# Kernel tuning notes

Measured on AMD Instinct MI355X. Metric: run time of the kernel, lower is better.

## Reference

```python
import jax, jax.numpy as jnp
import numpy as np

D_MODEL = 1024
NUM_HEADS = 16
HEAD_DIM = D_MODEL // NUM_HEADS


def setup_inputs() -> dict:
    key = jax.random.key(0)
    ks = jax.random.split(key, 11)
    B, S = 2, 2048
    s = 1.0 / np.sqrt(D_MODEL)
    return {
        "q": jax.random.normal(ks[0], (B, S, D_MODEL), jnp.float32),
        "k": jax.random.normal(ks[1], (B, S, D_MODEL), jnp.float32),
        "v": jax.random.normal(ks[2], (B, S, D_MODEL), jnp.float32),
        "Wq": jax.random.normal(ks[3], (D_MODEL, D_MODEL), jnp.float32) * s,
        "bq": jnp.zeros((D_MODEL,), jnp.float32),
        "Wk": jax.random.normal(ks[4], (D_MODEL, D_MODEL), jnp.float32) * s,
        "bk": jnp.zeros((D_MODEL,), jnp.float32),
        "Wv": jax.random.normal(ks[5], (D_MODEL, D_MODEL), jnp.float32) * s,
        "bv": jnp.zeros((D_MODEL,), jnp.float32),
        "Wo": jax.random.normal(ks[6], (D_MODEL, D_MODEL), jnp.float32) * s,
        "bo": jnp.zeros((D_MODEL,), jnp.float32),
    }


def _split_heads(x):
    B, S, _ = x.shape
    return x.reshape(B, S, NUM_HEADS, HEAD_DIM).transpose(0, 2, 1, 3)  # [B,H,S,Dh]


def reference(q, k, v, Wq, bq, Wk, bk, Wv, bv, Wo, bo):
    B, S, _ = q.shape
    qh = _split_heads(q @ Wq.T + bq)
    kh = _split_heads(k @ Wk.T + bk)
    vh = _split_heads(v @ Wv.T + bv)
    scale = 1.0 / jnp.sqrt(jnp.asarray(HEAD_DIM, qh.dtype))
    scores = jnp.einsum("bhqd,bhkd->bhqk", qh, kh) * scale  # [B,H,S,S]
    attn = jax.nn.softmax(scores, axis=-1)
    out = jnp.einsum("bhqk,bhkd->bhqd", attn, vh)
    out = out.transpose(0, 2, 1, 3).reshape(B, S, D_MODEL)
    return out @ Wo.T + bo
```

## Files before the change

### kernel.cpp

```cpp
#include <hip/hip_runtime.h>
#include <cstdint>
#include <cstddef>

#define DEVI __device__ __forceinline__

typedef short bf16x8 __attribute__((ext_vector_type(8)));
typedef short bf16x4 __attribute__((ext_vector_type(4)));
typedef float f32x4 __attribute__((ext_vector_type(4)));
typedef float f32x16 __attribute__((ext_vector_type(16)));
typedef unsigned short u16x4 __attribute__((ext_vector_type(4)));

constexpr int D_MODEL = 1024;
constexpr int HEADS = 16;
constexpr int DH = 64;
constexpr int SEQ = 2048;
constexpr int KDIM = 1024;

DEVI unsigned short f2bf(float f) {
  union { float f; unsigned u; } v; v.f = f;
  unsigned r = v.u + 0x7fffu + ((v.u >> 16) & 1u);
  return (unsigned short)(r >> 16);
}

DEVI unsigned pkbf(float a, float b) {
  return __builtin_amdgcn_perm(__float_as_uint(b), __float_as_uint(a), 0x07060302u);
}

DEVI void cp16(const void* g, void* l) {
  __builtin_amdgcn_global_load_lds(
      (const __attribute__((address_space(1))) void*)g,
      (__attribute__((address_space(3))) void*)l, 16, 0, 0);
}

#define BAR()        asm volatile("s_barrier" ::: "memory")
#define WAITVM(n)    asm volatile("s_waitcnt vmcnt(" #n ")" ::: "memory")

__global__ void __launch_bounds__(256) castall(
    const float* __restrict__ q, const float* __restrict__ k, const float* __restrict__ v,
    const float* __restrict__ Wq, const float* __restrict__ Wk,
    const float* __restrict__ Wv, const float* __restrict__ Wo,
    unsigned short* __restrict__ qb, unsigned short* __restrict__ kb, unsigned short* __restrict__ vb,
    unsigned short* __restrict__ Wqb, unsigned short* __restrict__ Wkb,
    unsigned short* __restrict__ Wvb, unsigned short* __restrict__ Wob) {
  int bid = blockIdx.x;
  const float* s; unsigned short* d; int off;
  if (bid < 12288) {
    int w = bid >> 12; off = bid & 4095;
    s = (w == 0) ? q : ((w == 1) ? k : v);
    d = (w == 0) ? qb : ((w == 1) ? kb : vb);
  } else {
    int w = (bid - 12288) >> 10; off = bid & 1023;
    s = (w == 0) ? Wq : ((w == 1) ? Wk : ((w == 2) ? Wv : Wo));
    d = (w == 0) ? Wqb : ((w == 1) ? Wkb : ((w == 2) ? Wvb : Wob));
  }
  int i = (off * 256 + threadIdx.x) * 4;
  float4 x = *(const float4*)(s + i);
  u16x4 o; o[0] = f2bf(x.x); o[1] = f2bf(x.y); o[2] = f2bf(x.z); o[3] = f2bf(x.w);
  *(u16x4*)(d + i) = o;
}

__global__ void __launch_bounds__(256) qkv_gemm(
    const unsigned short* __restrict__ qb, const unsigned short* __restrict__ kb,
    const unsigned short* __restrict__ vb,
    const unsigned short* __restrict__ Wqb, const unsigned short* __restrict__ Wkb,
    const unsigned short* __restrict__ Wvb,
    const float* __restrict__ bq, const float* __restrict__ bk, const float* __restrict__ bv,
    unsigned short* __restrict__ Qh, unsigned short* __restrict__ Kh,
    unsigned short* __restrict__ Vt, float qscale) {
  __shared__ unsigned short As[3][128 * 32];
  __shared__ unsigned short Bs[3][128 * 32];
  const int bid = blockIdx.x, seg = bid >> 8, inner = bid & 255;
  const int bm = inner & 31, bn = inner >> 5;
  const unsigned short* A = (seg == 0) ? qb : ((seg == 1) ? kb : vb);
  const unsigned short* W = (seg == 0) ? Wqb : ((seg == 1) ? Wkb : Wvb);
  const float* bias = (seg == 0) ? bq : ((seg == 1) ? bk : bv);
  unsigned short* O = (seg == 0) ? Qh : ((seg == 1) ? Kh : Vt);
  const float oscale = (seg == 0) ? qscale : 1.0f;
  const int mode = (seg == 2) ? 1 : 0;

  const int tid = threadIdx.x, lane = tid & 63, wave = tid >> 6;
  const int l16 = lane & 15, quad = lane >> 4;
  const int wm = (wave >> 1) * 64, wn = (wave & 1) * 64;
  const int sw = (l16 >> 1) & 3;
  f32x4 acc[4][4] = {};

  const int r0 = tid >> 2, p0 = tid & 3;
  const int c0 = (p0 ^ ((r0 >> 1) & 3)) * 8;
  const int r1 = (256 + tid) >> 2;
  const int c1 = (p0 ^ ((r1 >> 1) & 3)) * 8;
  const unsigned short* Arow0 = A + (size_t)(bm * 128 + r0) * KDIM + c0;
  const unsigned short* Arow1 = A + (size_t)(bm * 128 + r1) * KDIM + c1;
  const unsigned short* Wrow0 = W + (size_t)(bn * 128 + r0) * KDIM + c0;
  const unsigned short* Wrow1 = W + (size_t)(bn * 128 + r1) * KDIM + c1;

#define QKV_ISSUE(K0, P)                                    \
  do {                                                      \
    cp16(Arow0 + (K0), &As[P][tid * 8]);                    \
    cp16(Arow1 + (K0), &As[P][(256 + tid) * 8]);            \
    cp16(Wrow0 + (K0), &Bs[P][tid * 8]);                    \
    cp16(Wrow1 + (K0), &Bs[P][(256 + tid) * 8]);            \
  } while (0)

#define QKV_COMPUTE(P)                                                             \
  do {                                                                             \
    bf16x8 af[4], bfr[4];                                                          \
    _Pragma("unroll") for (int t = 0; t < 4; ++t)                                  \
        af[t] = *(const bf16x8*)&As[P][(wm + t * 16 + l16) * 32 + ((quad ^ sw) * 8)]; \
    _Pragma("unroll") for (int t = 0; t < 4; ++t)                                  \
        bfr[t] = *(const bf16x8*)&Bs[P][(wn + t * 16 + l16) * 32 + ((quad ^ sw) * 8)]; \
    _Pragma("unroll") for (int i = 0; i < 4; ++i)                                  \
        _Pragma("unroll") for (int j = 0; j < 4; ++j)                              \
            acc[i][j] = __builtin_amdgcn_mfma_f32_16x16x32_bf16(af[i], bfr[j],     \
                                                                acc[i][j], 0, 0, 0); \
  } while (0)

  QKV_ISSUE(0, 0);
  QKV_ISSUE(32, 1);
  for (int k = 0; k < 30; k += 3) {
    BAR(); QKV_ISSUE((k + 2) * 32, 2); WAITVM(8); BAR(); QKV_COMPUTE(0);
    BAR(); QKV_ISSUE((k + 3) * 32, 0); WAITVM(8); BAR(); QKV_COMPUTE(1);
    BAR(); QKV_ISSUE((k + 4) * 32, 1); WAITVM(8); BAR(); QKV_COMPUTE(2);
  }
  WAITVM(4); BAR(); QKV_COMPUTE(0);
  WAITVM(0); BAR(); QKV_COMPUTE(1);

#pragma unroll
  for (int i = 0; i < 4; ++i) {
#pragma unroll
    for (int j = 0; j < 4; ++j) {
      const int col = bn * 128 + wn + j * 16 + l16;
      const float bv = bias[col];
#pragma unroll
      for (int r = 0; r < 4; ++r) {
        const int row = bm * 128 + wm + i * 16 + quad * 4 + r;
        const float val = (acc[i][j][r] + bv) * oscale;
        const int b = row >> 11, s = row & (SEQ - 1);
        const int h = col >> 6, d = col & (DH - 1);
        size_t idx;
        if (mode == 0) idx = ((size_t)(b * HEADS + h) * SEQ + s) * DH + d;
        else           idx = ((size_t)(b * HEADS + h) * DH + d) * SEQ + s;
        O[idx] = f2bf(val);
      }
    }
  }
#undef QKV_ISSUE
#undef QKV_COMPUTE
}

__global__ void __launch_bounds__(256) out_gemm(const unsigned short* __restrict__ AO,
                                                const unsigned short* __restrict__ Wob,
                                                const float* __restrict__ bo,
                                                float* __restrict__ out) {
  __shared__ unsigned short As[3][64 * 32];
  __shared__ unsigned short Bs[3][128 * 32];
  const int bid = blockIdx.x, bm = bid & 63, bn = bid >> 6;
  const int tid = threadIdx.x, lane = tid & 63, wave = tid >> 6;
  const int l16 = lane & 15, quad = lane >> 4;
  const int wn = wave * 32;
  const int sw = (l16 >> 1) & 3;
  f32x4 acc[4][2] = {};

  const int ra = tid >> 2, pa = tid & 3;
  const int ca = (pa ^ ((ra >> 1) & 3)) * 8;
  const int r1 = (256 + tid) >> 2;
  const int c1 = (pa ^ ((r1 >> 1) & 3)) * 8;
  const unsigned short* Arow  = AO + (size_t)(bm * 64 + ra) * KDIM + ca;
  const unsigned short* Wrow0 = Wob + (size_t)(bn * 128 + ra) * KDIM + ca;
  const unsigned short* Wrow1 = Wob + (size_t)(bn * 128 + r1) * KDIM + c1;

#define OUT_ISSUE(K0, P)                                    \
  do {                                                      \
    cp16(Arow + (K0), &As[P][tid * 8]);                     \
    cp16(Wrow0 + (K0), &Bs[P][tid * 8]);                    \
    cp16(Wrow1 + (K0), &Bs[P][(256 + tid) * 8]);            \
  } while (0)

#define OUT_COMPUTE(P)                                                             \
  do {                                                                             \
    bf16x8 af[4], bfr[2];                                                          \
    _Pragma("unroll") for (int t = 0; t < 4; ++t)                                  \
        af[t] = *(const bf16x8*)&As[P][(t * 16 + l16) * 32 + ((quad ^ sw) * 8)];   \
    _Pragma("unroll") for (int u = 0; u < 2; ++u)                                  \
        bfr[u] = *(const bf16x8*)&Bs[P][(wn + u * 16 + l16) * 32 + ((quad ^ sw) * 8)]; \
    _Pragma("unroll") for (int i = 0; i < 4; ++i)                                  \
        _Pragma("unroll") for (int j = 0; j < 2; ++j)                              \
            acc[i][j] = __builtin_amdgcn_mfma_f32_16x16x32_bf16(af[i], bfr[j],     \
                                                                acc[i][j], 0, 0, 0); \
  } while (0)

  OUT_ISSUE(0, 0);
  OUT_ISSUE(32, 1);
  for (int k = 0; k < 30; k += 3) {
    BAR(); OUT_ISSUE((k + 2) * 32, 2); WAITVM(6); BAR(); OUT_COMPUTE(0);
    BAR(); OUT_ISSUE((k + 3) * 32, 0); WAITVM(6); BAR(); OUT_COMPUTE(1);
    BAR(); OUT_ISSUE((k + 4) * 32, 1); WAITVM(6); BAR(); OUT_COMPUTE(2);
  }
  WAITVM(3); BAR(); OUT_COMPUTE(0);
  WAITVM(0); BAR(); OUT_COMPUTE(1);

#pragma unroll
  for (int i = 0; i < 4; ++i)
#pragma unroll
    for (int j = 0; j < 2; ++j) {
      const int col = bn * 128 + wn + j * 16 + l16;
      const float bv = bo[col];
#pragma unroll
      for (int r = 0; r < 4; ++r) {
        const int row = bm * 64 + i * 16 + quad * 4 + r;
        out[(size_t)row * D_MODEL + col] = acc[i][j][r] + bv;
      }
    }
#undef OUT_ISSUE
#undef OUT_COMPUTE
}

__global__ void __launch_bounds__(256) attn(const unsigned short* __restrict__ Qh,
                                            const unsigned short* __restrict__ Kh,
                                            const unsigned short* __restrict__ Vt,
                                            unsigned short* __restrict__ AO) {
  __shared__ __align__(16) char smem[65536];

  const int bid = blockIdx.x;
  const int qt = bid >> 5, head = bid & 31, b = head >> 4, h = head & 15;
  const int tid = threadIdx.x;
  const int lane = tid & 63, wave = tid >> 6;
  const int wq = wave >> 1, wk = wave & 1;
  const int l31 = lane & 31, hh = lane >> 5;

  const unsigned short* Qhead = Qh + (size_t)(b * HEADS + h) * SEQ * DH;
  const unsigned short* Khead = Kh + (size_t)(b * HEADS + h) * SEQ * DH;
  const unsigned short* Vhead = Vt + (size_t)(b * HEADS + h) * DH * SEQ;

  const int qrow = qt * 64 + wq * 32 + l31;
  bf16x8 aq[4];
#pragma unroll
  for (int it = 0; it < 4; ++it)
    aq[it] = *(const bf16x8*)&Qhead[(size_t)qrow * DH + it * 16 + hh * 8];

  f32x16 oacc[2] = {};
  float lsum = 0.f;

  const int krow = tid >> 3, kpb = tid & 7;
  const int vd = tid >> 4, vpb = tid & 15;

#define ATT_STAGE(KC, P)                                                      \
  do {                                                                        \
    unsigned short* Ksp = (unsigned short*)(smem + (P) * 32768);              \
    unsigned short* Vsp = (unsigned short*)(smem + (P) * 32768 + 16384);      \
    _Pragma("unroll") for (int c = 0; c < 4; ++c) {                           \
      int row = c * 32 + krow;                                                \
      int jb = kpb ^ (row & 7);                                               \
      cp16(Khead + (size_t)((KC) * 128 + row) * DH + jb * 8,                  \
           &Ksp[(c * 256 + tid) * 8]);                                        \
    }                                                                         \
    _Pragma("unroll") for (int c = 0; c < 4; ++c) {                           \
      int d = c * 16 + vd;                                                    \
      int jb = vpb ^ (d & 7);                                                 \
      cp16(Vhead + (size_t)d * SEQ + (KC) * 128 + jb * 8,                     \
           &Vsp[(c * 256 + tid) * 8]);                                        \
    }                                                                         \
  } while (0)

#define ATT_COMPUTE(P)                                                        \
  do {                                                                        \
    const unsigned short* Ksp = (const unsigned short*)(smem + (P) * 32768);  \
    const unsigned short* Vsp =                                               \
        (const unsigned short*)(smem + (P) * 32768 + 16384);                  \
    __builtin_amdgcn_s_setprio(1);                                            \
    _Pragma("unroll") for (int sub = 0; sub < 2; ++sub) {                     \
      const int kb32 = sub * 64 + wk * 32;                                    \
      const int key = kb32 + l31;                                             \
      f32x16 sa = {};                                                         \
      _Pragma("unroll") for (int it = 0; it < 4; ++it) {                      \
        const int sblk = (2 * it + hh) ^ (key & 7);                           \
        bf16x8 ak = *(const bf16x8*)&Ksp[key * 64 + sblk * 8];                \
        sa = __builtin_amdgcn_mfma_f32_32x32x16_bf16(ak, aq[it], sa, 0, 0, 0);\
      }                                                                       \
      float p[16];                                                            \
      _Pragma("unroll") for (int r = 0; r < 16; ++r) {                        \
        p[r] = __builtin_amdgcn_exp2f(sa[r]);                                 \
        lsum += p[r];                                                         \
      }                                                                       \
      _Pragma("unroll") for (int c = 0; c < 2; ++c) {                         \
        unsigned x0 = pkbf(p[8 * c + 0], p[8 * c + 1]);                       \
        unsigned x1 = pkbf(p[8 * c + 2], p[8 * c + 3]);                       \
        unsigned y0 = pkbf(p[8 * c + 4], p[8 * c + 5]);                       \
        unsigned y1 = pkbf(p[8 * c + 6], p[8 * c + 7]);                       \
        asm("v_permlane32_swap_b32 %0, %1" : "+v"(x0), "+v"(y0));             \
        asm("v_permlane32_swap_b32 %0, %1" : "+v"(x1), "+v"(y1));             \
        union { unsigned u[4]; bf16x8 s; } pb;                                \
        pb.u[0] = x0; pb.u[1] = x1; pb.u[2] = y0; pb.u[3] = y1;               \
        const int K8 = sub * 8 + wk * 4 + 2 * c + hh;                         \
        _Pragma("unroll") for (int dh2 = 0; dh2 < 2; ++dh2) {                 \
          const int d = dh2 * 32 + l31;                                       \
          const int sv = K8 ^ (d & 7);                                        \
          bf16x8 av = *(const bf16x8*)&Vsp[d * 128 + sv * 8];                 \
          oacc[dh2] = __builtin_amdgcn_mfma_f32_32x32x16_bf16(av, pb.s,       \
                                                              oacc[dh2],     \
                                                              0, 0, 0);      \
        }                                                                     \
      }                                                                       \
    }                                                                         \
    __builtin_amdgcn_s_setprio(0);                                            \
  } while (0)

  ATT_STAGE(0, 0);
  for (int kc = 0; kc < 15; ++kc) {
    BAR();
    ATT_STAGE(kc + 1, (kc + 1) & 1);
    WAITVM(8);
    BAR();
    ATT_COMPUTE(kc & 1);
  }
  WAITVM(0);
  BAR();
  ATT_COMPUTE(1);

  lsum += __shfl_xor(lsum, 32);

  float* epiF = (float*)smem;
  float* lbuf = (float*)(smem + 16384);
  unsigned short* Oq = (unsigned short*)(smem + 17408);

  if (l31 == lane) lbuf[wave * 32 + l31] = lsum;
  if (wk == 1) {
#pragma unroll
    for (int dh2 = 0; dh2 < 2; ++dh2)
#pragma unroll
      for (int r = 0; r < 16; ++r) {
        const int d = dh2 * 32 + (r & 3) + 8 * (r >> 2) + 4 * hh;
        epiF[wq * 2048 + d * 32 + l31] = oacc[dh2][r];
      }
  }
  __syncthreads();

  if (wk == 0) {
    const float linv = 1.0f / (lsum + lbuf[(wq * 2 + 1) * 32 + l31]);
#pragma unroll
    for (int dh2 = 0; dh2 < 2; ++dh2) {
#pragma unroll
      for (int r = 0; r < 16; r += 2) {
        const int d = dh2 * 32 + (r & 3) + 8 * (r >> 2) + 4 * hh;
        const float v0 = (oacc[dh2][r]     + epiF[wq * 2048 + d * 32 + l31]) * linv;
        const float v1 = (oacc[dh2][r + 1] + epiF[wq * 2048 + (d + 1) * 32 + l31]) * linv;
        *(unsigned*)&Oq[wq * 2176 + l31 * 68 + d] = pkbf(v0, v1);
      }
    }
  }
  __syncthreads();

  {
    const int qloc = tid >> 2, d0 = (tid & 3) * 16;
    const int base = (qloc >> 5) * 2176 + (qloc & 31) * 68 + d0;
    unsigned u[8];
#pragma unroll
    for (int i = 0; i < 8; ++i) u[i] = *(const unsigned*)&Oq[base + i * 2];
    unsigned short* dst = AO + ((size_t)(b * SEQ + qt * 64 + qloc)) * D_MODEL + h * 64 + d0;
    *(uint4*)dst       = make_uint4(u[0], u[1], u[2], u[3]);
    *(uint4*)(dst + 8) = make_uint4(u[4], u[5], u[6], u[7]);
  }
#undef ATT_STAGE
#undef ATT_COMPUTE
}

extern "C" void kernel_launch(void* const* d_in, const int* in_sizes, int n_in,
                              void* d_out, int out_size, void* d_ws, size_t ws_size,
                              hipStream_t stream) {
  const float* q  = (const float*)d_in[0];
  const float* k  = (const float*)d_in[1];
  const float* v  = (const float*)d_in[2];
  const float* Wq = (const float*)d_in[3];
  const float* bq = (const float*)d_in[4];
  const float* Wk = (const float*)d_in[5];
  const float* bk = (const float*)d_in[6];
  const float* Wv = (const float*)d_in[7];
  const float* bv = (const float*)d_in[8];
  const float* Wo = (const float*)d_in[9];
  const float* bo = (const float*)d_in[10];
  float* out = (float*)d_out;

  char* ws = (char*)d_ws;
  const size_t MB = 1ull << 20;
  unsigned short* qb  = (unsigned short*)(ws + 0 * MB);
  unsigned short* kb  = (unsigned short*)(ws + 8 * MB);
  unsigned short* vb  = (unsigned short*)(ws + 16 * MB);
  unsigned short* Wqb = (unsigned short*)(ws + 24 * MB);
  unsigned short* Wkb = (unsigned short*)(ws + 26 * MB);
  unsigned short* Wvb = (unsigned short*)(ws + 28 * MB);
  unsigned short* Wob = (unsigned short*)(ws + 30 * MB);
  unsigned short* Qh  = (unsigned short*)(ws + 32 * MB);
  unsigned short* Kh  = (unsigned short*)(ws + 40 * MB);
  unsigned short* Vt  = (unsigned short*)(ws + 48 * MB);
  unsigned short* AO  = (unsigned short*)(ws + 56 * MB);

  castall<<<16384, 256, 0, stream>>>(q, k, v, Wq, Wk, Wv, Wo,
                                     qb, kb, vb, Wqb, Wkb, Wvb, Wob);

  const float qscale = 0.125f * 1.44269504088896f;
  qkv_gemm<<<768, 256, 0, stream>>>(qb, kb, vb, Wqb, Wkb, Wvb, bq, bk, bv,
                                    Qh, Kh, Vt, qscale);

  attn<<<1024, 256, 0, stream>>>(Qh, Kh, Vt, AO);

  out_gemm<<<512, 256, 0, stream>>>(AO, Wob, bo, out);
}
```

Measured before the change: 232.8 us.

## Double attention query tile per block to reuse K/V tiles across two query sets

Each block now handles 128 query rows instead of 64, and each wave computes two 32-row query sets against the same K and V fragments, halving K/V global traffic and LDS K loads per query. The grid is halved to 512 blocks with launch bounds of one block per SM, and the pipeline now waits for all loads before each compute and adds a trailing barrier. Register pressure roughly doubles for the accumulators, and the fully synchronous prefetch wait may expose load latency. Fewer blocks can also leave compute units underused.

```diff
diff --git a/kernel.cpp b/kernel.cpp
--- a/kernel.cpp
+++ b/kernel.cpp
@@ -214,10 +214,10 @@
 #undef OUT_COMPUTE
 }
 
-__global__ void __launch_bounds__(256) attn(const unsigned short* __restrict__ Qh,
-                                            const unsigned short* __restrict__ Kh,
-                                            const unsigned short* __restrict__ Vt,
-                                            unsigned short* __restrict__ AO) {
+__global__ void __launch_bounds__(256, 1) attn(const unsigned short* __restrict__ Qh,
+                                               const unsigned short* __restrict__ Kh,
+                                               const unsigned short* __restrict__ Vt,
+                                               unsigned short* __restrict__ AO) {
   __shared__ __align__(16) char smem[65536];
 
   const int bid = blockIdx.x;
@@ -231,33 +231,52 @@
   const unsigned short* Khead = Kh + (size_t)(b * HEADS + h) * SEQ * DH;
   const unsigned short* Vhead = Vt + (size_t)(b * HEADS + h) * DH * SEQ;
 
-  const int qrow = qt * 64 + wq * 32 + l31;
-  bf16x8 aq[4];
-#pragma unroll
-  for (int it = 0; it < 4; ++it)
-    aq[it] = *(const bf16x8*)&Qhead[(size_t)qrow * DH + it * 16 + hh * 8];
-
-  f32x16 oacc[2] = {};
-  float lsum = 0.f;
-
-  const int krow = tid >> 3, kpb = tid & 7;
-  const int vd = tid >> 4, vpb = tid & 15;
+  const int qrow0 = qt * 128 + wq * 64 + l31;
+  bf16x8 aq0[4], aq1[4];
+#pragma unroll
+  for (int it = 0; it < 4; ++it) {
+    aq0[it] = *(const bf16x8*)&Qhead[(size_t)qrow0 * DH + it * 16 + hh * 8];
+    aq1[it] = *(const bf16x8*)&Qhead[(size_t)(qrow0 + 32) * DH + it * 16 + hh * 8];
+  }
+
+  f32x16 oacc0[2] = {}, oacc1[2] = {};
+  float lsum0 = 0.f, lsum1 = 0.f;
 
 #define ATT_STAGE(KC, P)                                                      \
   do {                                                                        \
     unsigned short* Ksp = (unsigned short*)(smem + (P) * 32768);              \
     unsigned short* Vsp = (unsigned short*)(smem + (P) * 32768 + 16384);      \
     _Pragma("unroll") for (int c = 0; c < 4; ++c) {                           \
-      int row = c * 32 + krow;                                                \
-      int jb = kpb ^ (row & 7);                                               \
-      cp16(Khead + (size_t)((KC) * 128 + row) * DH + jb * 8,                  \
-           &Ksp[(c * 256 + tid) * 8]);                                        \
+      int s = c * 256 + tid;                                                  \
+      int row = s >> 3, pblk = s & 7;                                         \
+      int jb = pblk ^ (row & 7);                                              \
+      cp16(Khead + (size_t)((KC) * 128 + row) * DH + jb * 8, &Ksp[s * 8]);    \
     }                                                                         \
     _Pragma("unroll") for (int c = 0; c < 4; ++c) {                           \
-      int d = c * 16 + vd;                                                    \
-      int jb = vpb ^ (d & 7);                                                 \
-      cp16(Vhead + (size_t)d * SEQ + (KC) * 128 + jb * 8,                     \
-           &Vsp[(c * 256 + tid) * 8]);                                        \
+      int s = c * 256 + tid;                                                  \
+      int d = s >> 4, pblk = s & 15;                                          \
+      int jb = pblk ^ (d & 7);                                                \
+      cp16(Vhead + (size_t)d * SEQ + (KC) * 128 + jb * 8, &Vsp[s * 8]);       \
+    }                                                                         \
+  } while (0)
+
+#define ATT_SOFTMAX(SA, PB, LSUM)                                             \
+  do {                                                                        \
+    float p[16];                                                              \
+    _Pragma("unroll") for (int r = 0; r < 16; ++r) {                          \
+      p[r] = __builtin_amdgcn_exp2f((SA)[r]);                                 \
+      (LSUM) += p[r];                                                         \
+    }                                                                         \
+    _Pragma("unroll") for (int c = 0; c < 2; ++c) {                           \
+      unsigned x0 = pkbf(p[8 * c + 0], p[8 * c + 1]);                         \
+      unsigned x1 = pkbf(p[8 * c + 2], p[8 * c + 3]);                         \
+      unsigned y0 = pkbf(p[8 * c + 4], p[8 * c + 5]);                         \
+      unsigned y1 = pkbf(p[8 * c + 6], p[8 * c + 7]);                         \
+      asm("v_permlane32_swap_b32 %0, %1" : "+v"(x0), "+v"(y0));               \
+      asm("v_permlane32_swap_b32 %0, %1" : "+v"(x1), "+v"(y1));               \
+      union { unsigned u[4]; bf16x8 s; } pbu;                                 \
+      pbu.u[0] = x0; pbu.u[1] = x1; pbu.u[2] = y0; pbu.u[3] = y1;             \
+      (PB)[c] = pbu.s;                                                        \
     }                                                                         \
   } while (0)
 
@@ -268,36 +287,39 @@
         (const unsigned short*)(smem + (P) * 32768 + 16384);                  \
     __builtin_amdgcn_s_setprio(1);                                            \
     _Pragma("unroll") for (int sub = 0; sub < 2; ++sub) {                     \
-      const int kb32 = sub * 64 + wk * 32;                                    \
-      const int key = kb32 + l31;                                             \
-      f32x16 sa = {};                                                         \
+      const int key = sub * 64 + wk * 32 + l31;                               \
+      bf16x8 ak[4];                                                           \
       _Pragma("unroll") for (int it = 0; it < 4; ++it) {                      \
         const int sblk = (2 * it + hh) ^ (key & 7);                           \
-        bf16x8 ak = *(const bf16x8*)&Ksp[key * 64 + sblk * 8];                \
-        sa = __builtin_amdgcn_mfma_f32_32x32x16_bf16(ak, aq[it], sa, 0, 0, 0);\
+        ak[it] = *(const bf16x8*)&Ksp[key * 64 + sblk * 8];                   \
       }                                                                       \
-      float p[16];                                                            \
-      _Pragma("unroll") for (int r = 0; r < 16; ++r) {                        \
-        p[r] = __builtin_amdgcn_exp2f(sa[r]);                                 \
-        lsum += p[r];                                                         \
+      bf16x8 pb0[2], pb1[2];                                                  \
+      {                                                                       \
+        f32x16 sa = {};                                                       \
+        _Pragma("unroll") for (int it = 0; it < 4; ++it)                      \
+          sa = __builtin_amdgcn_mfma_f32_32x32x16_bf16(ak[it], aq0[it], sa,   \
+                                                       0, 0, 0);              \
+        ATT_SOFTMAX(sa, pb0, lsum0);                                          \
+      }                                                                       \
+      {                                                                       \
+        f32x16 sa = {};                                                       \
+        _Pragma("unroll") for (int it = 0; it < 4; ++it)                      \
+          sa = __builtin_amdgcn_mfma_f32_32x32x16_bf16(ak[it], aq1[it], sa,   \
+                                                       0, 0, 0);              \
+        ATT_SOFTMAX(sa, pb1, lsum1);                                          \
       }                                                                       \
       _Pragma("unroll") for (int c = 0; c < 2; ++c) {                         \
-        unsigned x0 = pkbf(p[8 * c + 0], p[8 * c + 1]);                       \
-        unsigned x1 = pkbf(p[8 * c + 2], p[8 * c + 3]);                       \
-        unsigned y0 = pkbf(p[8 * c + 4], p[8 * c + 5]);                       \
-        unsigned y1 = pkbf(p[8 * c + 6], p[8 * c + 7]);                       \
-        asm("v_permlane32_swap_b32 %0, %1" : "+v"(x0), "+v"(y0));             \
-        asm("v_permlane32_swap_b32 %0, %1" : "+v"(x1), "+v"(y1));             \
-        union { unsigned u[4]; bf16x8 s; } pb;                                \
-        pb.u[0] = x0; pb.u[1] = x1; pb.u[2] = y0; pb.u[3] = y1;               \
         const int K8 = sub * 8 + wk * 4 + 2 * c + hh;                         \
         _Pragma("unroll") for (int dh2 = 0; dh2 < 2; ++dh2) {                 \
           const int d = dh2 * 32 + l31;                                       \
           const int sv = K8 ^ (d & 7);                                        \
           bf16x8 av = *(const bf16x8*)&Vsp[d * 128 + sv * 8];                 \
-          oacc[dh2] = __builtin_amdgcn_mfma_f32_32x32x16_bf16(av, pb.s,       \
-                                                              oacc[dh2],     \
-                                                              0, 0, 0);      \
+          oacc0[dh2] = __builtin_amdgcn_mfma_f32_32x32x16_bf16(av, pb0[c],    \
+                                                               oacc0[dh2],   \
+                                                               0, 0, 0);     \
+          oacc1[dh2] = __builtin_amdgcn_mfma_f32_32x32x16_bf16(av, pb1[c],    \
+                                                               oacc1[dh2],   \
+                                                               0, 0, 0);     \
         }                                                                     \
       }                                                                       \
     }                                                                         \
@@ -305,62 +327,69 @@
   } while (0)
 
   ATT_STAGE(0, 0);
-  for (int kc = 0; kc < 15; ++kc) {
+  for (int kc = 0; kc < 16; ++kc) {
+    WAITVM(0);
     BAR();
-    ATT_STAGE(kc + 1, (kc + 1) & 1);
-    WAITVM(8);
+    if (kc < 15) ATT_STAGE(kc + 1, (kc + 1) & 1);
+    ATT_COMPUTE(kc & 1);
     BAR();
-    ATT_COMPUTE(kc & 1);
-  }
-  WAITVM(0);
-  BAR();
-  ATT_COMPUTE(1);
-
-  lsum += __shfl_xor(lsum, 32);
+  }
+
+  lsum0 += __shfl_xor(lsum0, 32);
+  lsum1 += __shfl_xor(lsum1, 32);
 
   float* epiF = (float*)smem;
   float* lbuf = (float*)(smem + 16384);
   unsigned short* Oq = (unsigned short*)(smem + 17408);
 
-  if (l31 == lane) lbuf[wave * 32 + l31] = lsum;
-  if (wk == 1) {
-#pragma unroll
-    for (int dh2 = 0; dh2 < 2; ++dh2)
-#pragma unroll
-      for (int r = 0; r < 16; ++r) {
-        const int d = dh2 * 32 + (r & 3) + 8 * (r >> 2) + 4 * hh;
-        epiF[wq * 2048 + d * 32 + l31] = oacc[dh2][r];
-      }
-  }
+#define ATT_EPI(OACC, LSUM, SET)                                              \
+  do {                                                                        \
+    if (lane < 32) lbuf[wave * 32 + l31] = (LSUM);                            \
+    if (wk == 1) {                                                            \
+      _Pragma("unroll") for (int dh2 = 0; dh2 < 2; ++dh2)                     \
+        _Pragma("unroll") for (int r = 0; r < 16; ++r) {                      \
+          const int d = dh2 * 32 + (r & 3) + 8 * (r >> 2) + 4 * hh;           \
+          epiF[wq * 2048 + d * 32 + l31] = (OACC)[dh2][r];                    \
+        }                                                                     \
+    }                                                                         \
+    __syncthreads();                                                          \
+    if (wk == 0) {                                                            \
+      const float linv = 1.0f / ((LSUM) + lbuf[(wq * 2 + 1) * 32 + l31]);     \
+      _Pragma("unroll") for (int dh2 = 0; dh2 < 2; ++dh2) {                   \
+        _Pragma("unroll") for (int r = 0; r < 16; r += 2) {                   \
+          const int d = dh2 * 32 + (r & 3) + 8 * (r >> 2) + 4 * hh;           \
+          const float v0 =                                                    \
+              ((OACC)[dh2][r] + epiF[wq * 2048 + d * 32 + l31]) * linv;       \
+          const float v1 =                                                    \
+              ((OACC)[dh2][r + 1] + epiF[wq * 2048 + (d + 1) * 32 + l31]) *   \
+              linv;                                                           \
+          *(unsigned*)&Oq[wq * 2176 + l31 * 68 + d] = pkbf(v0, v1);           \
+        }                                                                     \
+      }                                                                       \
+    }                                                                         \
+    __syncthreads();                                                          \
+    {                                                                         \
+      const int qloc = tid >> 2, d0 = (tid & 3) * 16;                         \
+      const int base = (qloc >> 5) * 2176 + (qloc & 31) * 68 + d0;            \
+      unsigned u[8];                                                          \
+      _Pragma("unroll") for (int i = 0; i < 8; ++i)                           \
+        u[i] = *(const unsigned*)&Oq[base + i * 2];                           \
+      const int row = qt * 128 + (qloc >> 5) * 64 + (SET) * 32 + (qloc & 31); \
+      unsigned short* dst =                                                   \
+          AO + ((size_t)(b * SEQ + row)) * D_MODEL + h * 64 + d0;             \
+      *(uint4*)dst       = make_uint4(u[0], u[1], u[2], u[3]);                \
+      *(uint4*)(dst + 8) = make_uint4(u[4], u[5], u[6], u[7]);                \
+    }                                                                         \
+  } while (0)
+
+  ATT_EPI(oacc0, lsum0, 0);
   __syncthreads();
-
-  if (wk == 0) {
-    const float linv = 1.0f / (lsum + lbuf[(wq * 2 + 1) * 32 + l31]);
-#pragma unroll
-    for (int dh2 = 0; dh2 < 2; ++dh2) {
-#pragma unroll
-      for (int r = 0; r < 16; r += 2) {
-        const int d = dh2 * 32 + (r & 3) + 8 * (r >> 2) + 4 * hh;
-        const float v0 = (oacc[dh2][r]     + epiF[wq * 2048 + d * 32 + l31]) * linv;
-        const float v1 = (oacc[dh2][r + 1] + epiF[wq * 2048 + (d + 1) * 32 + l31]) * linv;
-        *(unsigned*)&Oq[wq * 2176 + l31 * 68 + d] = pkbf(v0, v1);
-      }
-    }
-  }
-  __syncthreads();
-
-  {
-    const int qloc = tid >> 2, d0 = (tid & 3) * 16;
-    const int base = (qloc >> 5) * 2176 + (qloc & 31) * 68 + d0;
-    unsigned u[8];
-#pragma unroll
-    for (int i = 0; i < 8; ++i) u[i] = *(const unsigned*)&Oq[base + i * 2];
-    unsigned short* dst = AO + ((size_t)(b * SEQ + qt * 64 + qloc)) * D_MODEL + h * 64 + d0;
-    *(uint4*)dst       = make_uint4(u[0], u[1], u[2], u[3]);
-    *(uint4*)(dst + 8) = make_uint4(u[4], u[5], u[6], u[7]);
-  }
+  ATT_EPI(oacc1, lsum1, 1);
+
 #undef ATT_STAGE
+#undef ATT_SOFTMAX
 #undef ATT_COMPUTE
+#undef ATT_EPI
 }
 
 extern "C" void kernel_launch(void* const* d_in, const int* in_sizes, int n_in,
@@ -400,7 +429,7 @@
   qkv_gemm<<<768, 256, 0, stream>>>(qb, kb, vb, Wqb, Wkb, Wvb, bq, bk, bv,
                                     Qh, Kh, Vt, qscale);
 
-  attn<<<1024, 256, 0, stream>>>(Qh, Kh, Vt, AO);
+  attn<<<512, 256, 0, stream>>>(Qh, Kh, Vt, AO);
 
   out_gemm<<<512, 256, 0, stream>>>(AO, Wob, bo, out);
 }
```

Measured after the change: 223.5 us. 4.0% less time.
